# Kernel optimization log

Hardware: AMD Instinct MI355X
Metric: run time of the kernel (lower is better)

## Reference

```python
import jax, jax.numpy as jnp
import numpy as np

HEADS = 4
HEAD_DIM = 32
IN_DIM = 128
N_TRIG = 48
N_SPAN = 128


def build_edges(T, S):
    # nodes are (trig r, span c) flattened row-major: n = r*S + c
    N = T * S
    nodes = jnp.arange(N, dtype=jnp.int32)
    r = nodes // S
    c = nodes % S
    # same-row neighbors (includes self loop once): [N, S]
    row_nb = r[:, None] * S + jnp.arange(S, dtype=jnp.int32)[None, :]
    # same-column neighbors excluding own row: [N, T-1]
    t_idx = jnp.arange(T - 1, dtype=jnp.int32)[None, :]
    t = t_idx + (t_idx >= r[:, None]).astype(jnp.int32)
    col_nb = t * S + c[:, None]
    deg = S + T - 1
    src = jnp.concatenate([row_nb, col_nb], axis=1).reshape(-1)  # [N*deg]
    dst = jnp.repeat(nodes, deg)
    return src, dst, N


def gat_conv(x, src, dst, N, W, att_src, att_dst, bias):
    # PyG GATConv (eval mode, dropout off), concat=True.
    # W: [in, H*Hd]; att_src/att_dst: [H, Hd]; bias: [H*Hd]
    h = (x @ W).reshape(N, HEADS, HEAD_DIM)          # [N,H,Hd]
    a_src = jnp.sum(h * att_src[None], axis=-1)      # [N,H]
    a_dst = jnp.sum(h * att_dst[None], axis=-1)      # [N,H]
    e = jax.nn.leaky_relu(a_src[src] + a_dst[dst], negative_slope=0.2)  # [E,H]
    # scatter-softmax over incoming edges per destination node
    m = jax.ops.segment_max(e, dst, num_segments=N)  # [N,H]
    ex = jnp.exp(e - m[dst])
    denom = jax.ops.segment_sum(ex, dst, num_segments=N)
    alpha = ex / denom[dst]                          # [E,H]
    msg = alpha[:, :, None] * h[src]                 # [E,H,Hd]
    out = jax.ops.segment_sum(msg, dst, num_segments=N)  # [N,H,Hd]
    return out.reshape(N, HEADS * HEAD_DIM) + bias[None]


def setup_inputs() -> dict:
    key = jax.random.key(0)
    ks = jax.random.split(key, 9)
    D = IN_DIM
    HD = HEADS * HEAD_DIM
    inp = {
        "pair_embeddings": jax.random.normal(ks[0], (1, N_TRIG, N_SPAN, D), dtype=jnp.float32),
        "W1": jax.random.normal(ks[1], (D, HD), dtype=jnp.float32) * (2.0 / (D + HD)) ** 0.5,
        "att_src1": jax.random.normal(ks[2], (HEADS, HEAD_DIM), dtype=jnp.float32) * 0.1,
        "att_dst1": jax.random.normal(ks[3], (HEADS, HEAD_DIM), dtype=jnp.float32) * 0.1,
        "b1": jnp.zeros((HD,), dtype=jnp.float32),
        "W2": jax.random.normal(ks[4], (HD, HD), dtype=jnp.float32) * (2.0 / (HD + HD)) ** 0.5,
        "att_src2": jax.random.normal(ks[5], (HEADS, HEAD_DIM), dtype=jnp.float32) * 0.1,
        "att_dst2": jax.random.normal(ks[6], (HEADS, HEAD_DIM), dtype=jnp.float32) * 0.1,
        "b2": jnp.zeros((HD,), dtype=jnp.float32),
        "num_trigs_kept": N_TRIG,
        "num_arg_spans_kept": N_SPAN,
    }
    return inp


def reference(pair_embeddings, W1, att_src1, att_dst1, b1, W2, att_src2, att_dst2, b2, num_trigs_kept, num_arg_spans_kept):
    T, S = int(num_trigs_kept), int(num_arg_spans_kept)
    src, dst, N = build_edges(T, S)
    # batch_size == 1: slice and flatten node features
    x = pair_embeddings[0, :T, :S].reshape(N, -1)
    x = jax.nn.elu(gat_conv(x, src, dst, N, W1, att_src1, att_dst1, b1))
    x = jax.nn.elu(gat_conv(x, src, dst, N, W2, att_src2, att_dst2, b2))
    return x
```

## Files before the change

kernel.cpp:

```cpp
#include <hip/hip_runtime.h>

#define T_TRIG 48
#define S_SPAN 128
#define NN (T_TRIG * S_SPAN)
#define D 128

typedef __attribute__((ext_vector_type(8))) short sh8;
typedef __attribute__((ext_vector_type(4))) float f32x4;
typedef __attribute__((ext_vector_type(4))) unsigned short us4;

__device__ inline unsigned short f2bf(float v) {
    unsigned u = __float_as_uint(v);
    unsigned r = u + 0x7FFFu + ((u >> 16) & 1u);
    return (unsigned short)(r >> 16);
}
__device__ inline float bf2f(unsigned short b) {
    return __uint_as_float(((unsigned)b) << 16);
}

__global__ __launch_bounds__(256) void prep_kernel(
    const float* __restrict__ pe, const float* __restrict__ W1,
    const float* __restrict__ W2,
    unsigned short* __restrict__ x1h, unsigned short* __restrict__ x1l,
    unsigned short* __restrict__ w1h, unsigned short* __restrict__ w1l,
    unsigned short* __restrict__ w2h, unsigned short* __restrict__ w2l)
{
    const int b = blockIdx.x;
    const int t = threadIdx.x;
    if (b < 16) {
        const float* W = (b < 8) ? W1 : W2;
        unsigned short* wh = (b < 8) ? w1h : w2h;
        unsigned short* wl = (b < 8) ? w1l : w2l;
        const int nt = b & 7;
        const int kc = t >> 6;
        const int l = t & 63;
        const int n = nt * 16 + (l & 15);
        const int kb = kc * 32 + (l >> 4) * 8;
        unsigned short hb[8], lb[8];
        #pragma unroll
        for (int i = 0; i < 8; ++i) {
            float v = W[(kb + i) * D + n];
            unsigned short h = f2bf(v);
            hb[i] = h;
            lb[i] = f2bf(v - bf2f(h));
        }
        size_t base = ((size_t)(nt * 4 + kc) * 64 + l) * 8;
        #pragma unroll
        for (int i = 0; i < 8; ++i) { wh[base + i] = hb[i]; wl[base + i] = lb[i]; }
    } else {
        const int idx = (b - 16) * 256 + t;
        const float* p = pe + (size_t)idx * 8;
        float4 v0 = *(const float4*)p;
        float4 v1 = *(const float4*)(p + 4);
        float xs[8] = {v0.x, v0.y, v0.z, v0.w, v1.x, v1.y, v1.z, v1.w};
        sh8 hv, lv;
        #pragma unroll
        for (int i = 0; i < 8; ++i) {
            unsigned short h = f2bf(xs[i]);
            hv[i] = (short)h;
            lv[i] = (short)f2bf(xs[i] - bf2f(h));
        }
        ((sh8*)x1h)[idx] = hv;
        ((sh8*)x1l)[idx] = lv;
    }
}

__global__ __launch_bounds__(256) void gemm_mfma_kernel(
    const unsigned short* __restrict__ Xh, const unsigned short* __restrict__ Xl,
    const unsigned short* __restrict__ Wh, const unsigned short* __restrict__ Wl,
    const float* __restrict__ att_s, const float* __restrict__ att_d,
    float* __restrict__ H, float* __restrict__ asrc, float* __restrict__ adst)
{
    __shared__ float ps_part[4][16], pd_part[4][16];

    const int t = threadIdx.x;
    const int w = t >> 6;
    const int l = t & 63;
    const int mt = blockIdx.x >> 1;
    const int nq = blockIdx.x & 1;
    const int nt = nq * 4 + w;
    const int c = l & 15;
    const int kg = l >> 4;
    const int row0 = mt * 16;

    const sh8* Xh8 = (const sh8*)Xh;
    const sh8* Xl8 = (const sh8*)Xl;
    const sh8* Wh8 = (const sh8*)Wh;
    const sh8* Wl8 = (const sh8*)Wl;

    f32x4 acc = {0, 0, 0, 0};
    #pragma unroll
    for (int kc = 0; kc < 4; ++kc) {
        const int xi = (row0 + c) * 16 + kc * 4 + kg;
        sh8 ah = Xh8[xi];
        sh8 al = Xl8[xi];
        sh8 bh = Wh8[(nt * 4 + kc) * 64 + l];
        sh8 bl = Wl8[(nt * 4 + kc) * 64 + l];
        acc = __builtin_amdgcn_mfma_f32_16x16x32_bf16(ah, bh, acc, 0, 0, 0);
        acc = __builtin_amdgcn_mfma_f32_16x16x32_bf16(al, bh, acc, 0, 0, 0);
        acc = __builtin_amdgcn_mfma_f32_16x16x32_bf16(ah, bl, acc, 0, 0, 0);
    }

    #pragma unroll
    for (int i = 0; i < 4; ++i)
        H[(size_t)(row0 + kg * 4 + i) * D + nt * 16 + c] = acc[i];

    const int dim = (nt >> 1) * 32 + (nt & 1) * 16 + c;
    const float asv = att_s[dim];
    const float adv = att_d[dim];
    #pragma unroll
    for (int i = 0; i < 4; ++i) {
        float ps = acc[i] * asv;
        float pd = acc[i] * adv;
        ps += __shfl_xor(ps, 1); pd += __shfl_xor(pd, 1);
        ps += __shfl_xor(ps, 2); pd += __shfl_xor(pd, 2);
        ps += __shfl_xor(ps, 4); pd += __shfl_xor(pd, 4);
        ps += __shfl_xor(ps, 8); pd += __shfl_xor(pd, 8);
        if (c == 0) {
            ps_part[w][kg * 4 + i] = ps;
            pd_part[w][kg * 4 + i] = pd;
        }
    }
    __syncthreads();
    if (t < 32) {
        const int row = t & 15;
        const int hh = t >> 4;
        const int head = nq * 2 + hh;
        asrc[(row0 + row) * 4 + head] = ps_part[2 * hh][row] + ps_part[2 * hh + 1][row];
        adst[(row0 + row) * 4 + head] = pd_part[2 * hh][row] + pd_part[2 * hh + 1][row];
    }
}

__global__ __launch_bounds__(256) void row_agg_kernel(
    const float* __restrict__ H, const float* __restrict__ asrc,
    const float* __restrict__ adst, float* __restrict__ num_row,
    float* __restrict__ den_row)
{
    __shared__ float sh_h[S_SPAN][32];
    __shared__ float sh_as[S_SPAN];
    const int tid = threadIdx.x;
    const int r = blockIdx.x >> 2;
    const int h = blockIdx.x & 3;
    const int base = r * S_SPAN;

    #pragma unroll
    for (int it = 0; it < 4; ++it) {
        int chunk = tid + it * 256;
        int cp = chunk >> 3, fc = chunk & 7;
        *(float4*)&sh_h[cp][fc * 4] =
            *(const float4*)&H[(size_t)(base + cp) * D + h * 32 + fc * 4];
    }
    if (tid < S_SPAN) sh_as[tid] = asrc[(base + tid) * 4 + h];
    __syncthreads();

    const int fg = tid & 3;
    const int cth = tid >> 2;
    const float ad0 = adst[(base + cth) * 4 + h];
    const float ad1 = adst[(base + cth + 64) * 4 + h];
    float4 n00 = {0,0,0,0}, n01 = {0,0,0,0}, n10 = {0,0,0,0}, n11 = {0,0,0,0};
    float den0 = 0.f, den1 = 0.f;

    #pragma unroll 2
    for (int cp = 0; cp < S_SPAN; ++cp) {
        float a = sh_as[cp];
        float4 h0 = *(float4*)&sh_h[cp][fg * 8];
        float4 h1 = *(float4*)&sh_h[cp][fg * 8 + 4];
        float e0 = a + ad0; e0 = fmaxf(e0, 0.2f * e0);
        float e1 = a + ad1; e1 = fmaxf(e1, 0.2f * e1);
        float w0 = __expf(e0);
        float w1 = __expf(e1);
        den0 += w0; den1 += w1;
        n00.x = fmaf(w0, h0.x, n00.x); n00.y = fmaf(w0, h0.y, n00.y);
        n00.z = fmaf(w0, h0.z, n00.z); n00.w = fmaf(w0, h0.w, n00.w);
        n01.x = fmaf(w0, h1.x, n01.x); n01.y = fmaf(w0, h1.y, n01.y);
        n01.z = fmaf(w0, h1.z, n01.z); n01.w = fmaf(w0, h1.w, n01.w);
        n10.x = fmaf(w1, h0.x, n10.x); n10.y = fmaf(w1, h0.y, n10.y);
        n10.z = fmaf(w1, h0.z, n10.z); n10.w = fmaf(w1, h0.w, n10.w);
        n11.x = fmaf(w1, h1.x, n11.x); n11.y = fmaf(w1, h1.y, n11.y);
        n11.z = fmaf(w1, h1.z, n11.z); n11.w = fmaf(w1, h1.w, n11.w);
    }

    const int n0 = base + cth, n1 = n0 + 64;
    *(float4*)&num_row[(size_t)n0 * D + h * 32 + fg * 8]     = n00;
    *(float4*)&num_row[(size_t)n0 * D + h * 32 + fg * 8 + 4] = n01;
    *(float4*)&num_row[(size_t)n1 * D + h * 32 + fg * 8]     = n10;
    *(float4*)&num_row[(size_t)n1 * D + h * 32 + fg * 8 + 4] = n11;
    if (fg == 0) {
        den_row[n0 * 4 + h] = den0;
        den_row[n1 * 4 + h] = den1;
    }
}

__global__ __launch_bounds__(256) void col_agg_kernel(
    const float* __restrict__ H, const float* __restrict__ asrc,
    const float* __restrict__ adst, const float* __restrict__ num_row,
    const float* __restrict__ den_row, const float* __restrict__ bias,
    float* __restrict__ out, unsigned short* __restrict__ xh,
    unsigned short* __restrict__ xl)
{
    __shared__ float sh_h[T_TRIG][D];
    __shared__ float sh_as[4][T_TRIG];
    const int c = blockIdx.x;
    const int tid = threadIdx.x;

    #pragma unroll
    for (int it = 0; it < 6; ++it) {
        int chunk = tid + it * 256;
        int t = chunk >> 5, fc = chunk & 31;
        *(float4*)&sh_h[t][fc * 4] =
            *(const float4*)&H[(size_t)(t * S_SPAN + c) * D + fc * 4];
    }
    if (tid < 4 * T_TRIG) {
        int hh = tid / T_TRIG, t = tid - hh * T_TRIG;
        sh_as[hh][t] = asrc[(t * S_SPAN + c) * 4 + hh];
    }
    __syncthreads();

    const int f4g = tid & 31;
    const int tg = tid >> 5;
    const int head = f4g >> 3;

    float4 num[6];
    float den[6], ad[6];
    #pragma unroll
    for (int dd = 0; dd < 6; ++dd) {
        num[dd] = {0,0,0,0};
        den[dd] = 0.f;
        ad[dd] = adst[((tg * 6 + dd) * S_SPAN + c) * 4 + head];
    }

    for (int tp = 0; tp < T_TRIG; ++tp) {
        float a = sh_as[head][tp];
        float4 hv = *(float4*)&sh_h[tp][f4g * 4];
        #pragma unroll
        for (int dd = 0; dd < 6; ++dd) {
            float e = a + ad[dd];
            e = fmaxf(e, 0.2f * e);
            float w = __expf(e);
            w = (tp == tg * 6 + dd) ? 0.f : w;
            den[dd] += w;
            num[dd].x = fmaf(w, hv.x, num[dd].x);
            num[dd].y = fmaf(w, hv.y, num[dd].y);
            num[dd].z = fmaf(w, hv.z, num[dd].z);
            num[dd].w = fmaf(w, hv.w, num[dd].w);
        }
    }

    const float4 b4 = *(const float4*)&bias[f4g * 4];
    #pragma unroll
    for (int dd = 0; dd < 6; ++dd) {
        int n = (tg * 6 + dd) * S_SPAN + c;
        float4 nr = *(const float4*)&num_row[(size_t)n * D + f4g * 4];
        float dr = den_row[n * 4 + head];
        float inv = 1.f / (dr + den[dd]);
        float o[4];
        o[0] = (nr.x + num[dd].x) * inv + b4.x;
        o[1] = (nr.y + num[dd].y) * inv + b4.y;
        o[2] = (nr.z + num[dd].z) * inv + b4.z;
        o[3] = (nr.w + num[dd].w) * inv + b4.w;
        #pragma unroll
        for (int q = 0; q < 4; ++q)
            o[q] = o[q] > 0.f ? o[q] : (__expf(o[q]) - 1.f);
        if (xh) {
            us4 hv4, lv4;
            #pragma unroll
            for (int q = 0; q < 4; ++q) {
                unsigned short hq = f2bf(o[q]);
                hv4[q] = hq;
                lv4[q] = f2bf(o[q] - bf2f(hq));
            }
            *(us4*)&xh[(size_t)n * D + f4g * 4] = hv4;
            *(us4*)&xl[(size_t)n * D + f4g * 4] = lv4;
        } else {
            float4 o4 = {o[0], o[1], o[2], o[3]};
            *(float4*)&out[(size_t)n * D + f4g * 4] = o4;
        }
    }
}

extern "C" void kernel_launch(void* const* d_in, const int* in_sizes, int n_in,
                              void* d_out, int out_size, void* d_ws, size_t ws_size,
                              hipStream_t stream)
{
    const float* pe  = (const float*)d_in[0];
    const float* W1  = (const float*)d_in[1];
    const float* as1 = (const float*)d_in[2];
    const float* ad1 = (const float*)d_in[3];
    const float* b1  = (const float*)d_in[4];
    const float* W2  = (const float*)d_in[5];
    const float* as2 = (const float*)d_in[6];
    const float* ad2 = (const float*)d_in[7];
    const float* b2  = (const float*)d_in[8];
    float* out = (float*)d_out;

    char* ws = (char*)d_ws;
    float* H     = (float*)ws;
    float* numr  = H + (size_t)NN * D;
    float* asrcb = numr + (size_t)NN * D;
    float* adstb = asrcb + (size_t)NN * 4;
    float* denb  = adstb + (size_t)NN * 4;
    unsigned short* x1h = (unsigned short*)(denb + (size_t)NN * 4);
    unsigned short* x1l = x1h + (size_t)NN * D;
    unsigned short* x2h = x1l + (size_t)NN * D;
    unsigned short* x2l = x2h + (size_t)NN * D;
    unsigned short* w1h = x2l + (size_t)NN * D;
    unsigned short* w1l = w1h + D * D;
    unsigned short* w2h = w1l + D * D;
    unsigned short* w2l = w2h + D * D;

    prep_kernel<<<dim3(16 + NN * D / 8 / 256), dim3(256), 0, stream>>>(
        pe, W1, W2, x1h, x1l, w1h, w1l, w2h, w2l);

    gemm_mfma_kernel<<<dim3(NN / 16 * 2), dim3(256), 0, stream>>>(
        x1h, x1l, w1h, w1l, as1, ad1, H, asrcb, adstb);
    row_agg_kernel<<<dim3(T_TRIG * 4), dim3(256), 0, stream>>>(H, asrcb, adstb, numr, denb);
    col_agg_kernel<<<dim3(S_SPAN), dim3(256), 0, stream>>>(
        H, asrcb, adstb, numr, denb, b1, nullptr, x2h, x2l);
    gemm_mfma_kernel<<<dim3(NN / 16 * 2), dim3(256), 0, stream>>>(
        x2h, x2l, w2h, w2l, as2, ad2, H, asrcb, adstb);
    row_agg_kernel<<<dim3(T_TRIG * 4), dim3(256), 0, stream>>>(H, asrcb, adstb, numr, denb);
    col_agg_kernel<<<dim3(S_SPAN), dim3(256), 0, stream>>>(
        H, asrcb, adstb, numr, denb, b2, out, nullptr, nullptr);
}
```

Measured before the change: 81.57 us.

## Fuse all GAT stages into one persistent kernel with grid barriers

Replaces the seven kernel launches with a single 384-block kernel that runs layer-1 GEMM, row aggregation, column aggregation, layer-2 GEMM and both aggregations in sequence, separated by atomic-counter grid barriers. The input bf16 hi/lo split now happens inside the first GEMM, so the separate prep pass and its buffers go away, and the W2 split is done by the last blocks of stage one. Row and column work is re-partitioned so all 384 blocks share each stage. The aim is to remove launch gaps and the prep memory traffic. The cost is spin-barrier overhead, a memset per call, and a dependence on all 384 blocks being co-resident.

```diff
diff --git a/kernel.cpp b/kernel.cpp
--- a/kernel.cpp
+++ b/kernel.cpp
@@ -4,6 +4,7 @@
 #define S_SPAN 128
 #define NN (T_TRIG * S_SPAN)
 #define D 128
+#define GRID 384
 
 typedef __attribute__((ext_vector_type(8))) short sh8;
 typedef __attribute__((ext_vector_type(4))) float f32x4;
@@ -18,227 +19,232 @@
     return __uint_as_float(((unsigned)b) << 16);
 }
 
-__global__ __launch_bounds__(256) void prep_kernel(
-    const float* __restrict__ pe, const float* __restrict__ W1,
-    const float* __restrict__ W2,
-    unsigned short* __restrict__ x1h, unsigned short* __restrict__ x1l,
-    unsigned short* __restrict__ w1h, unsigned short* __restrict__ w1l,
-    unsigned short* __restrict__ w2h, unsigned short* __restrict__ w2l)
-{
-    const int b = blockIdx.x;
-    const int t = threadIdx.x;
-    if (b < 16) {
-        const float* W = (b < 8) ? W1 : W2;
-        unsigned short* wh = (b < 8) ? w1h : w2h;
-        unsigned short* wl = (b < 8) ? w1l : w2l;
-        const int nt = b & 7;
-        const int kc = t >> 6;
-        const int l = t & 63;
-        const int n = nt * 16 + (l & 15);
-        const int kb = kc * 32 + (l >> 4) * 8;
-        unsigned short hb[8], lb[8];
-        #pragma unroll
-        for (int i = 0; i < 8; ++i) {
-            float v = W[(kb + i) * D + n];
-            unsigned short h = f2bf(v);
-            hb[i] = h;
-            lb[i] = f2bf(v - bf2f(h));
-        }
-        size_t base = ((size_t)(nt * 4 + kc) * 64 + l) * 8;
-        #pragma unroll
-        for (int i = 0; i < 8; ++i) { wh[base + i] = hb[i]; wl[base + i] = lb[i]; }
-    } else {
-        const int idx = (b - 16) * 256 + t;
-        const float* p = pe + (size_t)idx * 8;
-        float4 v0 = *(const float4*)p;
-        float4 v1 = *(const float4*)(p + 4);
-        float xs[8] = {v0.x, v0.y, v0.z, v0.w, v1.x, v1.y, v1.z, v1.w};
-        sh8 hv, lv;
-        #pragma unroll
-        for (int i = 0; i < 8; ++i) {
-            unsigned short h = f2bf(xs[i]);
-            hv[i] = (short)h;
-            lv[i] = (short)f2bf(xs[i] - bf2f(h));
-        }
-        ((sh8*)x1h)[idx] = hv;
-        ((sh8*)x1l)[idx] = lv;
-    }
-}
-
-__global__ __launch_bounds__(256) void gemm_mfma_kernel(
-    const unsigned short* __restrict__ Xh, const unsigned short* __restrict__ Xl,
-    const unsigned short* __restrict__ Wh, const unsigned short* __restrict__ Wl,
-    const float* __restrict__ att_s, const float* __restrict__ att_d,
-    float* __restrict__ H, float* __restrict__ asrc, float* __restrict__ adst)
-{
-    __shared__ float ps_part[4][16], pd_part[4][16];
-
-    const int t = threadIdx.x;
-    const int w = t >> 6;
-    const int l = t & 63;
-    const int mt = blockIdx.x >> 1;
-    const int nq = blockIdx.x & 1;
-    const int nt = nq * 4 + w;
-    const int c = l & 15;
-    const int kg = l >> 4;
-    const int row0 = mt * 16;
-
-    const sh8* Xh8 = (const sh8*)Xh;
-    const sh8* Xl8 = (const sh8*)Xl;
-    const sh8* Wh8 = (const sh8*)Wh;
-    const sh8* Wl8 = (const sh8*)Wl;
-
-    f32x4 acc = {0, 0, 0, 0};
-    #pragma unroll
-    for (int kc = 0; kc < 4; ++kc) {
-        const int xi = (row0 + c) * 16 + kc * 4 + kg;
-        sh8 ah = Xh8[xi];
-        sh8 al = Xl8[xi];
-        sh8 bh = Wh8[(nt * 4 + kc) * 64 + l];
-        sh8 bl = Wl8[(nt * 4 + kc) * 64 + l];
-        acc = __builtin_amdgcn_mfma_f32_16x16x32_bf16(ah, bh, acc, 0, 0, 0);
-        acc = __builtin_amdgcn_mfma_f32_16x16x32_bf16(al, bh, acc, 0, 0, 0);
-        acc = __builtin_amdgcn_mfma_f32_16x16x32_bf16(ah, bl, acc, 0, 0, 0);
-    }
-
-    #pragma unroll
-    for (int i = 0; i < 4; ++i)
-        H[(size_t)(row0 + kg * 4 + i) * D + nt * 16 + c] = acc[i];
-
-    const int dim = (nt >> 1) * 32 + (nt & 1) * 16 + c;
-    const float asv = att_s[dim];
-    const float adv = att_d[dim];
+struct Params {
+    const float *pe, *W1, *as1, *ad1, *b1, *W2, *as2, *ad2, *b2;
+    float* out;
+    unsigned int* bar;
+    unsigned short *x2h, *x2l, *w2h, *w2l;
+    float *H, *numr, *asrc, *adst, *den;
+};
+
+__device__ inline void gridbar(unsigned int* bar, unsigned int target) {
+    __syncthreads();
+    if (threadIdx.x == 0) {
+        __threadfence();
+        atomicAdd(bar, 1u);
+        while (atomicAdd(bar, 0u) < target)
+            __builtin_amdgcn_s_sleep(1);
+        __threadfence();
+    }
+    __syncthreads();
+}
+
+__device__ inline void store_epi(float* H, float* asrc, float* adst,
+                                 const float* att_s, const float* att_d,
+                                 const f32x4& a0, const f32x4& a1,
+                                 int row0, int hp, int c, int kg)
+{
     #pragma unroll
     for (int i = 0; i < 4; ++i) {
-        float ps = acc[i] * asv;
-        float pd = acc[i] * adv;
+        H[(size_t)(row0 + kg * 4 + i) * D + hp * 32 + c]      = a0[i];
+        H[(size_t)(row0 + kg * 4 + i) * D + hp * 32 + 16 + c] = a1[i];
+    }
+    const float as0 = att_s[hp * 32 + c],  as1v = att_s[hp * 32 + 16 + c];
+    const float ad0 = att_d[hp * 32 + c],  ad1v = att_d[hp * 32 + 16 + c];
+    #pragma unroll
+    for (int i = 0; i < 4; ++i) {
+        float ps = a0[i] * as0 + a1[i] * as1v;
+        float pd = a0[i] * ad0 + a1[i] * ad1v;
         ps += __shfl_xor(ps, 1); pd += __shfl_xor(pd, 1);
         ps += __shfl_xor(ps, 2); pd += __shfl_xor(pd, 2);
         ps += __shfl_xor(ps, 4); pd += __shfl_xor(pd, 4);
         ps += __shfl_xor(ps, 8); pd += __shfl_xor(pd, 8);
         if (c == 0) {
-            ps_part[w][kg * 4 + i] = ps;
-            pd_part[w][kg * 4 + i] = pd;
-        }
-    }
-    __syncthreads();
-    if (t < 32) {
-        const int row = t & 15;
-        const int hh = t >> 4;
-        const int head = nq * 2 + hh;
-        asrc[(row0 + row) * 4 + head] = ps_part[2 * hh][row] + ps_part[2 * hh + 1][row];
-        adst[(row0 + row) * 4 + head] = pd_part[2 * hh][row] + pd_part[2 * hh + 1][row];
-    }
-}
-
-__global__ __launch_bounds__(256) void row_agg_kernel(
-    const float* __restrict__ H, const float* __restrict__ asrc,
-    const float* __restrict__ adst, float* __restrict__ num_row,
-    float* __restrict__ den_row)
-{
-    __shared__ float sh_h[S_SPAN][32];
-    __shared__ float sh_as[S_SPAN];
-    const int tid = threadIdx.x;
-    const int r = blockIdx.x >> 2;
-    const int h = blockIdx.x & 3;
+            int rr = row0 + kg * 4 + i;
+            asrc[rr * 4 + hp] = ps;
+            adst[rr * 4 + hp] = pd;
+        }
+    }
+}
+
+__device__ void gemm_l1(const Params& p, int b, int t)
+{
+    const int w = t >> 6, l = t & 63;
+    const int c = l & 15, kg = l >> 4;
+    const int row0 = b * 16;
+    const int nt0 = w * 2, nt1 = nt0 + 1;
+
+    f32x4 a0 = {0,0,0,0}, a1 = {0,0,0,0};
+    #pragma unroll
+    for (int kc = 0; kc < 4; ++kc) {
+        const float* xp = p.pe + (size_t)(row0 + c) * D + kc * 32 + kg * 8;
+        float4 x0 = *(const float4*)xp;
+        float4 x1 = *(const float4*)(xp + 4);
+        float xs[8] = {x0.x, x0.y, x0.z, x0.w, x1.x, x1.y, x1.z, x1.w};
+        sh8 ah, al;
+        #pragma unroll
+        for (int i = 0; i < 8; ++i) {
+            unsigned short h = f2bf(xs[i]);
+            ah[i] = (short)h;
+            al[i] = (short)f2bf(xs[i] - bf2f(h));
+        }
+        const int kb = kc * 32 + kg * 8;
+        sh8 b0h, b0l, b1h, b1l;
+        #pragma unroll
+        for (int i = 0; i < 8; ++i) {
+            float v0 = p.W1[(size_t)(kb + i) * D + nt0 * 16 + c];
+            float v1 = p.W1[(size_t)(kb + i) * D + nt1 * 16 + c];
+            unsigned short h0 = f2bf(v0);
+            b0h[i] = (short)h0; b0l[i] = (short)f2bf(v0 - bf2f(h0));
+            unsigned short h1 = f2bf(v1);
+            b1h[i] = (short)h1; b1l[i] = (short)f2bf(v1 - bf2f(h1));
+        }
+        a0 = __builtin_amdgcn_mfma_f32_16x16x32_bf16(ah, b0h, a0, 0, 0, 0);
+        a0 = __builtin_amdgcn_mfma_f32_16x16x32_bf16(al, b0h, a0, 0, 0, 0);
+        a0 = __builtin_amdgcn_mfma_f32_16x16x32_bf16(ah, b0l, a0, 0, 0, 0);
+        a1 = __builtin_amdgcn_mfma_f32_16x16x32_bf16(ah, b1h, a1, 0, 0, 0);
+        a1 = __builtin_amdgcn_mfma_f32_16x16x32_bf16(al, b1h, a1, 0, 0, 0);
+        a1 = __builtin_amdgcn_mfma_f32_16x16x32_bf16(ah, b1l, a1, 0, 0, 0);
+    }
+    store_epi(p.H, p.asrc, p.adst, p.as1, p.ad1, a0, a1, row0, w, c, kg);
+
+    if (b >= GRID - 8) {
+        const int nt = b - (GRID - 8);
+        const int kc = t >> 6;
+        const int ll = t & 63;
+        const int n = nt * 16 + (ll & 15);
+        const int kb = kc * 32 + (ll >> 4) * 8;
+        unsigned short hb[8], lb[8];
+        #pragma unroll
+        for (int i = 0; i < 8; ++i) {
+            float v = p.W2[(size_t)(kb + i) * D + n];
+            unsigned short h = f2bf(v);
+            hb[i] = h;
+            lb[i] = f2bf(v - bf2f(h));
+        }
+        size_t base = ((size_t)(nt * 4 + kc) * 64 + ll) * 8;
+        #pragma unroll
+        for (int i = 0; i < 8; ++i) { p.w2h[base + i] = hb[i]; p.w2l[base + i] = lb[i]; }
+    }
+}
+
+__device__ void gemm_l2(const Params& p, int b, int t)
+{
+    const int w = t >> 6, l = t & 63;
+    const int c = l & 15, kg = l >> 4;
+    const int row0 = b * 16;
+    const int nt0 = w * 2, nt1 = nt0 + 1;
+
+    const sh8* Xh8 = (const sh8*)p.x2h;
+    const sh8* Xl8 = (const sh8*)p.x2l;
+    const sh8* Wh8 = (const sh8*)p.w2h;
+    const sh8* Wl8 = (const sh8*)p.w2l;
+
+    f32x4 a0 = {0,0,0,0}, a1 = {0,0,0,0};
+    #pragma unroll
+    for (int kc = 0; kc < 4; ++kc) {
+        const int xi = (row0 + c) * 16 + kc * 4 + kg;
+        sh8 ah = Xh8[xi];
+        sh8 al = Xl8[xi];
+        sh8 b0h = Wh8[(nt0 * 4 + kc) * 64 + l];
+        sh8 b0l = Wl8[(nt0 * 4 + kc) * 64 + l];
+        sh8 b1h = Wh8[(nt1 * 4 + kc) * 64 + l];
+        sh8 b1l = Wl8[(nt1 * 4 + kc) * 64 + l];
+        a0 = __builtin_amdgcn_mfma_f32_16x16x32_bf16(ah, b0h, a0, 0, 0, 0);
+        a0 = __builtin_amdgcn_mfma_f32_16x16x32_bf16(al, b0h, a0, 0, 0, 0);
+        a0 = __builtin_amdgcn_mfma_f32_16x16x32_bf16(ah, b0l, a0, 0, 0, 0);
+        a1 = __builtin_amdgcn_mfma_f32_16x16x32_bf16(ah, b1h, a1, 0, 0, 0);
+        a1 = __builtin_amdgcn_mfma_f32_16x16x32_bf16(al, b1h, a1, 0, 0, 0);
+        a1 = __builtin_amdgcn_mfma_f32_16x16x32_bf16(ah, b1l, a1, 0, 0, 0);
+    }
+    store_epi(p.H, p.asrc, p.adst, p.as2, p.ad2, a0, a1, row0, w, c, kg);
+}
+
+__device__ void do_row(const float* H, const float* asrc, const float* adst,
+                       float* numr, float* den, float* sm, int b, int t)
+{
+    float (*sh_h)[32] = (float(*)[32])sm;
+    float* sh_as = sm + 128 * 32;
+    const int r = b >> 3, sub = b & 7;
+    const int h = sub >> 1, half = sub & 1;
     const int base = r * S_SPAN;
 
     #pragma unroll
     for (int it = 0; it < 4; ++it) {
-        int chunk = tid + it * 256;
+        int chunk = t + it * 256;
         int cp = chunk >> 3, fc = chunk & 7;
         *(float4*)&sh_h[cp][fc * 4] =
             *(const float4*)&H[(size_t)(base + cp) * D + h * 32 + fc * 4];
     }
-    if (tid < S_SPAN) sh_as[tid] = asrc[(base + tid) * 4 + h];
-    __syncthreads();
-
-    const int fg = tid & 3;
-    const int cth = tid >> 2;
-    const float ad0 = adst[(base + cth) * 4 + h];
-    const float ad1 = adst[(base + cth + 64) * 4 + h];
-    float4 n00 = {0,0,0,0}, n01 = {0,0,0,0}, n10 = {0,0,0,0}, n11 = {0,0,0,0};
-    float den0 = 0.f, den1 = 0.f;
-
-    #pragma unroll 2
+    if (t < 128) sh_as[t] = asrc[(base + t) * 4 + h];
+    __syncthreads();
+
+    const int fg = t & 3;
+    const int cc = half * 64 + (t >> 2);
+    const float ad = adst[(base + cc) * 4 + h];
+    float4 n0 = {0,0,0,0}, n1 = {0,0,0,0};
+    float dn = 0.f;
+
+    #pragma unroll 4
     for (int cp = 0; cp < S_SPAN; ++cp) {
-        float a = sh_as[cp];
+        float e = sh_as[cp] + ad;
+        e = fmaxf(e, 0.2f * e);
+        float wgt = __expf(e);
+        dn += wgt;
         float4 h0 = *(float4*)&sh_h[cp][fg * 8];
         float4 h1 = *(float4*)&sh_h[cp][fg * 8 + 4];
-        float e0 = a + ad0; e0 = fmaxf(e0, 0.2f * e0);
-        float e1 = a + ad1; e1 = fmaxf(e1, 0.2f * e1);
-        float w0 = __expf(e0);
-        float w1 = __expf(e1);
-        den0 += w0; den1 += w1;
-        n00.x = fmaf(w0, h0.x, n00.x); n00.y = fmaf(w0, h0.y, n00.y);
-        n00.z = fmaf(w0, h0.z, n00.z); n00.w = fmaf(w0, h0.w, n00.w);
-        n01.x = fmaf(w0, h1.x, n01.x); n01.y = fmaf(w0, h1.y, n01.y);
-        n01.z = fmaf(w0, h1.z, n01.z); n01.w = fmaf(w0, h1.w, n01.w);
-        n10.x = fmaf(w1, h0.x, n10.x); n10.y = fmaf(w1, h0.y, n10.y);
-        n10.z = fmaf(w1, h0.z, n10.z); n10.w = fmaf(w1, h0.w, n10.w);
-        n11.x = fmaf(w1, h1.x, n11.x); n11.y = fmaf(w1, h1.y, n11.y);
-        n11.z = fmaf(w1, h1.z, n11.z); n11.w = fmaf(w1, h1.w, n11.w);
-    }
-
-    const int n0 = base + cth, n1 = n0 + 64;
-    *(float4*)&num_row[(size_t)n0 * D + h * 32 + fg * 8]     = n00;
-    *(float4*)&num_row[(size_t)n0 * D + h * 32 + fg * 8 + 4] = n01;
-    *(float4*)&num_row[(size_t)n1 * D + h * 32 + fg * 8]     = n10;
-    *(float4*)&num_row[(size_t)n1 * D + h * 32 + fg * 8 + 4] = n11;
-    if (fg == 0) {
-        den_row[n0 * 4 + h] = den0;
-        den_row[n1 * 4 + h] = den1;
-    }
-}
-
-__global__ __launch_bounds__(256) void col_agg_kernel(
-    const float* __restrict__ H, const float* __restrict__ asrc,
-    const float* __restrict__ adst, const float* __restrict__ num_row,
-    const float* __restrict__ den_row, const float* __restrict__ bias,
-    float* __restrict__ out, unsigned short* __restrict__ xh,
-    unsigned short* __restrict__ xl)
-{
-    __shared__ float sh_h[T_TRIG][D];
-    __shared__ float sh_as[4][T_TRIG];
-    const int c = blockIdx.x;
-    const int tid = threadIdx.x;
+        n0.x = fmaf(wgt, h0.x, n0.x); n0.y = fmaf(wgt, h0.y, n0.y);
+        n0.z = fmaf(wgt, h0.z, n0.z); n0.w = fmaf(wgt, h0.w, n0.w);
+        n1.x = fmaf(wgt, h1.x, n1.x); n1.y = fmaf(wgt, h1.y, n1.y);
+        n1.z = fmaf(wgt, h1.z, n1.z); n1.w = fmaf(wgt, h1.w, n1.w);
+    }
+
+    const int n = base + cc;
+    *(float4*)&numr[(size_t)n * D + h * 32 + fg * 8]     = n0;
+    *(float4*)&numr[(size_t)n * D + h * 32 + fg * 8 + 4] = n1;
+    if (fg == 0) den[n * 4 + h] = dn;
+    __syncthreads();
+}
+
+__device__ void do_col(const float* H, const float* asrc, const float* adst,
+                       const float* numr, const float* den, const float* bias,
+                       float* outf, unsigned short* xh, unsigned short* xl,
+                       float* sm, int b, int t)
+{
+    float (*sh_h)[D] = (float(*)[D])sm;
+    float (*sh_as)[T_TRIG] = (float(*)[T_TRIG])(sm + T_TRIG * D);
+    const int c = b & 127, third = b >> 7;
 
     #pragma unroll
     for (int it = 0; it < 6; ++it) {
-        int chunk = tid + it * 256;
-        int t = chunk >> 5, fc = chunk & 31;
-        *(float4*)&sh_h[t][fc * 4] =
-            *(const float4*)&H[(size_t)(t * S_SPAN + c) * D + fc * 4];
-    }
-    if (tid < 4 * T_TRIG) {
-        int hh = tid / T_TRIG, t = tid - hh * T_TRIG;
-        sh_as[hh][t] = asrc[(t * S_SPAN + c) * 4 + hh];
-    }
-    __syncthreads();
-
-    const int f4g = tid & 31;
-    const int tg = tid >> 5;
-    const int head = f4g >> 3;
-
-    float4 num[6];
-    float den[6], ad[6];
-    #pragma unroll
-    for (int dd = 0; dd < 6; ++dd) {
-        num[dd] = {0,0,0,0};
-        den[dd] = 0.f;
-        ad[dd] = adst[((tg * 6 + dd) * S_SPAN + c) * 4 + head];
-    }
+        int chunk = t + it * 256;
+        int tt = chunk >> 5, fc = chunk & 31;
+        *(float4*)&sh_h[tt][fc * 4] =
+            *(const float4*)&H[(size_t)(tt * S_SPAN + c) * D + fc * 4];
+    }
+    if (t < 4 * T_TRIG) {
+        int hh = t / T_TRIG, tt = t - hh * T_TRIG;
+        sh_as[hh][tt] = asrc[(tt * S_SPAN + c) * 4 + hh];
+    }
+    __syncthreads();
+
+    const int f4g = t & 31, tg = t >> 5, head = f4g >> 3;
+    const int t0 = third * 16 + tg * 2;
+    float4 num[2] = {{0,0,0,0},{0,0,0,0}};
+    float dn[2] = {0.f, 0.f};
+    float ad[2] = { adst[(t0 * S_SPAN + c) * 4 + head],
+                    adst[((t0 + 1) * S_SPAN + c) * 4 + head] };
 
     for (int tp = 0; tp < T_TRIG; ++tp) {
         float a = sh_as[head][tp];
         float4 hv = *(float4*)&sh_h[tp][f4g * 4];
         #pragma unroll
-        for (int dd = 0; dd < 6; ++dd) {
+        for (int dd = 0; dd < 2; ++dd) {
             float e = a + ad[dd];
             e = fmaxf(e, 0.2f * e);
             float w = __expf(e);
-            w = (tp == tg * 6 + dd) ? 0.f : w;
-            den[dd] += w;
+            w = (tp == t0 + dd) ? 0.f : w;
+            dn[dd] += w;
             num[dd].x = fmaf(w, hv.x, num[dd].x);
             num[dd].y = fmaf(w, hv.y, num[dd].y);
             num[dd].z = fmaf(w, hv.z, num[dd].z);
@@ -248,11 +254,10 @@
 
     const float4 b4 = *(const float4*)&bias[f4g * 4];
     #pragma unroll
-    for (int dd = 0; dd < 6; ++dd) {
-        int n = (tg * 6 + dd) * S_SPAN + c;
-        float4 nr = *(const float4*)&num_row[(size_t)n * D + f4g * 4];
-        float dr = den_row[n * 4 + head];
-        float inv = 1.f / (dr + den[dd]);
+    for (int dd = 0; dd < 2; ++dd) {
+        const int n = (t0 + dd) * S_SPAN + c;
+        float4 nr = *(const float4*)&numr[(size_t)n * D + f4g * 4];
+        float inv = 1.f / (den[n * 4 + head] + dn[dd]);
         float o[4];
         o[0] = (nr.x + num[dd].x) * inv + b4.x;
         o[1] = (nr.y + num[dd].y) * inv + b4.y;
@@ -273,52 +278,60 @@
             *(us4*)&xl[(size_t)n * D + f4g * 4] = lv4;
         } else {
             float4 o4 = {o[0], o[1], o[2], o[3]};
-            *(float4*)&out[(size_t)n * D + f4g * 4] = o4;
-        }
-    }
+            *(float4*)&outf[(size_t)n * D + f4g * 4] = o4;
+        }
+    }
+    __syncthreads();
+}
+
+__global__ __launch_bounds__(256, 2) void fused_gat_kernel(Params p)
+{
+    __shared__ float sm[T_TRIG * D + 4 * T_TRIG];
+    const int b = blockIdx.x, t = threadIdx.x;
+
+    gemm_l1(p, b, t);
+    gridbar(p.bar, 1 * GRID);
+    do_row(p.H, p.asrc, p.adst, p.numr, p.den, sm, b, t);
+    gridbar(p.bar, 2 * GRID);
+    do_col(p.H, p.asrc, p.adst, p.numr, p.den, p.b1, nullptr, p.x2h, p.x2l, sm, b, t);
+    gridbar(p.bar, 3 * GRID);
+    gemm_l2(p, b, t);
+    gridbar(p.bar, 4 * GRID);
+    do_row(p.H, p.asrc, p.adst, p.numr, p.den, sm, b, t);
+    gridbar(p.bar, 5 * GRID);
+    do_col(p.H, p.asrc, p.adst, p.numr, p.den, p.b2, p.out, nullptr, nullptr, sm, b, t);
 }
 
 extern "C" void kernel_launch(void* const* d_in, const int* in_sizes, int n_in,
                               void* d_out, int out_size, void* d_ws, size_t ws_size,
                               hipStream_t stream)
 {
-    const float* pe  = (const float*)d_in[0];
-    const float* W1  = (const float*)d_in[1];
-    const float* as1 = (const float*)d_in[2];
-    const float* ad1 = (const float*)d_in[3];
-    const float* b1  = (const float*)d_in[4];
-    const float* W2  = (const float*)d_in[5];
-    const float* as2 = (const float*)d_in[6];
-    const float* ad2 = (const float*)d_in[7];
-    const float* b2  = (const float*)d_in[8];
-    float* out = (float*)d_out;
+    Params p;
+    p.pe  = (const float*)d_in[0];
+    p.W1  = (const float*)d_in[1];
+    p.as1 = (const float*)d_in[2];
+    p.ad1 = (const float*)d_in[3];
+    p.b1  = (const float*)d_in[4];
+    p.W2  = (const float*)d_in[5];
+    p.as2 = (const float*)d_in[6];
+    p.ad2 = (const float*)d_in[7];
+    p.b2  = (const float*)d_in[8];
+    p.out = (float*)d_out;
 
     char* ws = (char*)d_ws;
-    float* H     = (float*)ws;
-    float* numr  = H + (size_t)NN * D;
-    float* asrcb = numr + (size_t)NN * D;
-    float* adstb = asrcb + (size_t)NN * 4;
-    float* denb  = adstb + (size_t)NN * 4;
-    unsigned short* x1h = (unsigned short*)(denb + (size_t)NN * 4);
-    unsigned short* x1l = x1h + (size_t)NN * D;
-    unsigned short* x2h = x1l + (size_t)NN * D;
-    unsigned short* x2l = x2h + (size_t)NN * D;
-    unsigned short* w1h = x2l + (size_t)NN * D;
-    unsigned short* w1l = w1h + D * D;
-    unsigned short* w2h = w1l + D * D;
-    unsigned short* w2l = w2h + D * D;
-
-    prep_kernel<<<dim3(16 + NN * D / 8 / 256), dim3(256), 0, stream>>>(
-        pe, W1, W2, x1h, x1l, w1h, w1l, w2h, w2l);
-
-    gemm_mfma_kernel<<<dim3(NN / 16 * 2), dim3(256), 0, stream>>>(
-        x1h, x1l, w1h, w1l, as1, ad1, H, asrcb, adstb);
-    row_agg_kernel<<<dim3(T_TRIG * 4), dim3(256), 0, stream>>>(H, asrcb, adstb, numr, denb);
-    col_agg_kernel<<<dim3(S_SPAN), dim3(256), 0, stream>>>(
-        H, asrcb, adstb, numr, denb, b1, nullptr, x2h, x2l);
-    gemm_mfma_kernel<<<dim3(NN / 16 * 2), dim3(256), 0, stream>>>(
-        x2h, x2l, w2h, w2l, as2, ad2, H, asrcb, adstb);
-    row_agg_kernel<<<dim3(T_TRIG * 4), dim3(256), 0, stream>>>(H, asrcb, adstb, numr, denb);
-    col_agg_kernel<<<dim3(S_SPAN), dim3(256), 0, stream>>>(
-        H, asrcb, adstb, numr, denb, b2, out, nullptr, nullptr);
-}
+    size_t off = 0;
+    auto alloc = [&](size_t bytes) { char* r = ws + off; off += (bytes + 255) & ~255ull; return r; };
+    p.bar  = (unsigned int*)alloc(256);
+    p.x2h  = (unsigned short*)alloc((size_t)NN * D * 2);
+    p.x2l  = (unsigned short*)alloc((size_t)NN * D * 2);
+    p.w2h  = (unsigned short*)alloc((size_t)D * D * 2);
+    p.w2l  = (unsigned short*)alloc((size_t)D * D * 2);
+    p.H    = (float*)alloc((size_t)NN * D * 4);
+    p.numr = (float*)alloc((size_t)NN * D * 4);
+    p.asrc = (float*)alloc((size_t)NN * 4 * 4);
+    p.adst = (float*)alloc((size_t)NN * 4 * 4);
+    p.den  = (float*)alloc((size_t)NN * 4 * 4);
+
+    hipMemsetAsync(p.bar, 0, 256, stream);
+    fused_gat_kernel<<<dim3(GRID), dim3(256), 0, stream>>>(p);
+}
```

Result: slower. 308.2 us (+277.8%).
